# Kernel optimization log

Measured on AMD Instinct MI355X. Metric: run time of the kernel, lower is better.

## Reference

```python
import jax, jax.numpy as jnp
import numpy as np

T, B, C, H, K = 2048, 4, 1024, 16, 7  # timesteps, batch, channels, heads, kernel
R = C // H  # channels per head


def setup_inputs() -> dict:
    key = jax.random.key(0)
    k1, k2 = jax.random.split(key)
    x = jax.random.normal(k1, (T, B, C), dtype=jnp.float32)
    # xavier_uniform for weight_linear: shape (H*K, C), fan_in=C, fan_out=H*K
    a = float(np.sqrt(6.0 / (C + H * K)))
    W = jax.random.uniform(k2, (H * K, C), dtype=jnp.float32, minval=-a, maxval=a)
    conv_bias = jnp.zeros((C,), dtype=jnp.float32)
    return {"x": x, "W": W, "conv_bias": conv_bias}


def reference(x, W, conv_bias):
    Tn, Bn, Cn = x.shape
    Kn, Hn = K, H
    Rn = Cn // Hn
    # dynamic filters predicted from the input itself (query = x)
    w = jnp.einsum('tbc,oc->tbo', x, W).reshape(Tn, Bn, Hn, Kn)
    w = jax.nn.softmax(w, axis=-1)  # softmax over the small kernel dim
    # causal unfold: padding_l = K-1 zeros on the left of the time axis
    x_pad = jnp.pad(x, ((Kn - 1, 0), (0, 0), (0, 0)))
    # x_unf[t, b, c, k] = x[t - (K-1) + k]  (zeros outside)
    x_unf = jnp.stack([x_pad[k:k + Tn] for k in range(Kn)], axis=-1)  # T,B,C,K
    x_unf = x_unf.reshape(Tn, Bn, Hn, Rn, Kn)
    out = jnp.einsum('tbhrk,tbhk->tbhr', x_unf, w).reshape(Tn, Bn, Cn)
    return out + conv_bias[None, None, :]
```

## Files before the change

kernel.cpp:

```cpp
#include <hip/hip_runtime.h>
#include <hip/hip_bf16.h>

#define T_DIM 2048
#define B_DIM 4
#define C_DIM 1024
#define H_DIM 16
#define K_DIM 7
#define HK    112

typedef float f32x4 __attribute__((ext_vector_type(4)));
typedef short s16x8 __attribute__((ext_vector_type(8)));

__device__ __forceinline__ short f2bf(float f) {
    union { float f; unsigned u; } v; v.f = f;
    return (short)((v.u + 0x7FFFu + ((v.u >> 16) & 1u)) >> 16);
}

__global__ void k_cvtW(const float* __restrict__ W, short* __restrict__ Wb) {
    const int i = ((int)blockIdx.x * 256 + (int)threadIdx.x) * 8;
    f32x4 a = *(const f32x4*)(W + i);
    f32x4 b = *(const f32x4*)(W + i + 4);
    s16x8 o;
    o[0] = f2bf(a[0]); o[1] = f2bf(a[1]); o[2] = f2bf(a[2]); o[3] = f2bf(a[3]);
    o[4] = f2bf(b[0]); o[5] = f2bf(b[1]); o[6] = f2bf(b[2]); o[7] = f2bf(b[3]);
    *(s16x8*)(Wb + i) = o;
}

__global__ __launch_bounds__(256) void k_fused(const float* __restrict__ x,
                                               const short* __restrict__ Wb,
                                               const float* __restrict__ bias,
                                               float* __restrict__ out) {
    __shared__ float sm[4][16][113];
    __shared__ float smw[16][HK];

    const int tid  = (int)threadIdx.x;
    const int lane = tid & 63;
    const int wid  = tid >> 6;
    const int m0   = (int)blockIdx.x * 16;
    const int t0   = (int)blockIdx.x * 4;

    const int cl   = lane & 15;
    const int koff = (lane >> 4) * 8;

    const float* aptr = x  + (size_t)(m0 + cl) * C_DIM + koff;
    const short* bptr = Wb + (size_t)cl * C_DIM + koff;

    f32x4 acc[K_DIM];
    #pragma unroll
    for (int n = 0; n < K_DIM; ++n) acc[n] = (f32x4){0.f, 0.f, 0.f, 0.f};

    for (int q = 0; q < 8; ++q) {
        const int kb = wid * 8 + q;
        f32x4 a0 = *(const f32x4*)(aptr + kb * 32);
        f32x4 a1 = *(const f32x4*)(aptr + kb * 32 + 4);
        s16x8 afr;
        afr[0] = f2bf(a0[0]); afr[1] = f2bf(a0[1]); afr[2] = f2bf(a0[2]); afr[3] = f2bf(a0[3]);
        afr[4] = f2bf(a1[0]); afr[5] = f2bf(a1[1]); afr[6] = f2bf(a1[2]); afr[7] = f2bf(a1[3]);
        #pragma unroll
        for (int nt = 0; nt < K_DIM; ++nt) {
            s16x8 bf = *(const s16x8*)(bptr + nt * 16 * C_DIM + kb * 32);
            acc[nt] = __builtin_amdgcn_mfma_f32_16x16x32_bf16(afr, bf, acc[nt], 0, 0, 0);
        }
    }

    const int r0 = (lane >> 4) * 4;
    #pragma unroll
    for (int nt = 0; nt < K_DIM; ++nt)
        #pragma unroll
        for (int j = 0; j < 4; ++j)
            sm[wid][r0 + j][nt * 16 + cl] = acc[nt][j];
    __syncthreads();

    {
        const int r = tid >> 4, h = tid & 15;
        float v[K_DIM];
        float mx = -1e30f;
        #pragma unroll
        for (int k = 0; k < K_DIM; ++k) {
            v[k] = sm[0][r][h * 7 + k] + sm[1][r][h * 7 + k]
                 + sm[2][r][h * 7 + k] + sm[3][r][h * 7 + k];
            mx = fmaxf(mx, v[k]);
        }
        float s = 0.f;
        #pragma unroll
        for (int k = 0; k < K_DIM; ++k) { v[k] = __expf(v[k] - mx); s += v[k]; }
        const float inv = 1.f / s;
        #pragma unroll
        for (int k = 0; k < K_DIM; ++k) smw[r][h * 7 + k] = v[k] * inv;
    }
    __syncthreads();

    const int c4 = tid * 4;
    const int h  = tid >> 4;
    const f32x4 bias4 = *(const f32x4*)(bias + c4);
    const f32x4 zero4 = {0.f, 0.f, 0.f, 0.f};

    #pragma unroll
    for (int b = 0; b < B_DIM; ++b) {
        f32x4 rv[10];
        #pragma unroll
        for (int j = 0; j < 10; ++j) {
            const int t = t0 - 6 + j;
            rv[j] = (t >= 0)
                  ? *(const f32x4*)(x + (size_t)(t * B_DIM + b) * C_DIM + c4)
                  : zero4;
        }
        #pragma unroll
        for (int tt = 0; tt < 4; ++tt) {
            const float* wr = &smw[tt * 4 + b][h * 7];
            f32x4 o = bias4;
            o += rv[tt + 0] * wr[0];
            o += rv[tt + 1] * wr[1];
            o += rv[tt + 2] * wr[2];
            o += rv[tt + 3] * wr[3];
            o += rv[tt + 4] * wr[4];
            o += rv[tt + 5] * wr[5];
            o += rv[tt + 6] * wr[6];
            *(f32x4*)(out + (size_t)((t0 + tt) * B_DIM + b) * C_DIM + c4) = o;
        }
    }
}

extern "C" void kernel_launch(void* const* d_in, const int* in_sizes, int n_in,
                              void* d_out, int out_size, void* d_ws, size_t ws_size,
                              hipStream_t stream) {
    const float* x    = (const float*)d_in[0];
    const float* W    = (const float*)d_in[1];
    const float* bias = (const float*)d_in[2];
    float* out = (float*)d_out;
    short* Wb  = (short*)d_ws;

    k_cvtW <<<56, 256, 0, stream>>>(W, Wb);
    k_fused<<<(T_DIM * B_DIM) / 16, 256, 0, stream>>>(x, Wb, bias, out);
}
```

Baseline: 111.5 us.

## Use 512-thread blocks with split-K over 8 waves and early prefetch of conv inputs

The block grows from 256 to 512 threads, so the K-reduction of the filter GEMM is split across 8 waves instead of 4, with an 8-way shared-memory reduction. In the conv phase each half of the block handles two batch entries instead of one thread looping over all four. The first batch's 10-step input window is loaded before the GEMM to hide its latency, while the second is loaded after the softmax. The aim is more parallelism per block and overlap of global loads with MFMA work, at the cost of higher register pressure and more shared memory.

```diff
diff --git a/kernel.cpp b/kernel.cpp
--- a/kernel.cpp
+++ b/kernel.cpp
@@ -26,11 +26,11 @@
     *(s16x8*)(Wb + i) = o;
 }
 
-__global__ __launch_bounds__(256) void k_fused(const float* __restrict__ x,
-                                               const short* __restrict__ Wb,
-                                               const float* __restrict__ bias,
-                                               float* __restrict__ out) {
-    __shared__ float sm[4][16][113];
+__global__ __launch_bounds__(512, 4) void k_fused(const float* __restrict__ x,
+                                                  const short* __restrict__ Wb,
+                                                  const float* __restrict__ bias,
+                                                  float* __restrict__ out) {
+    __shared__ float sm[8][16][113];
     __shared__ float smw[16][HK];
 
     const int tid  = (int)threadIdx.x;
@@ -38,6 +38,21 @@
     const int wid  = tid >> 6;
     const int m0   = (int)blockIdx.x * 16;
     const int t0   = (int)blockIdx.x * 4;
+
+    const int cid = tid & 255;
+    const int bs2 = (tid >> 8) * 2;
+    const int c4  = cid * 4;
+    const int h   = cid >> 4;
+    const f32x4 zero4 = {0.f, 0.f, 0.f, 0.f};
+
+    f32x4 rv0[10];
+    #pragma unroll
+    for (int j = 0; j < 10; ++j) {
+        const int t = t0 - 6 + j;
+        rv0[j] = (t >= 0)
+               ? *(const f32x4*)(x + (size_t)(t * B_DIM + bs2) * C_DIM + c4)
+               : zero4;
+    }
 
     const int cl   = lane & 15;
     const int koff = (lane >> 4) * 8;
@@ -49,16 +64,16 @@
     #pragma unroll
     for (int n = 0; n < K_DIM; ++n) acc[n] = (f32x4){0.f, 0.f, 0.f, 0.f};
 
-    for (int q = 0; q < 8; ++q) {
-        const int kb = wid * 8 + q;
-        f32x4 a0 = *(const f32x4*)(aptr + kb * 32);
-        f32x4 a1 = *(const f32x4*)(aptr + kb * 32 + 4);
+    for (int q = 0; q < 4; ++q) {
+        const int kb32 = (wid * 4 + q) * 32;
+        f32x4 a0 = *(const f32x4*)(aptr + kb32);
+        f32x4 a1 = *(const f32x4*)(aptr + kb32 + 4);
         s16x8 afr;
         afr[0] = f2bf(a0[0]); afr[1] = f2bf(a0[1]); afr[2] = f2bf(a0[2]); afr[3] = f2bf(a0[3]);
         afr[4] = f2bf(a1[0]); afr[5] = f2bf(a1[1]); afr[6] = f2bf(a1[2]); afr[7] = f2bf(a1[3]);
         #pragma unroll
         for (int nt = 0; nt < K_DIM; ++nt) {
-            s16x8 bf = *(const s16x8*)(bptr + nt * 16 * C_DIM + kb * 32);
+            s16x8 bf = *(const s16x8*)(bptr + nt * 16 * C_DIM + kb32);
             acc[nt] = __builtin_amdgcn_mfma_f32_16x16x32_bf16(afr, bf, acc[nt], 0, 0, 0);
         }
     }
@@ -71,14 +86,15 @@
             sm[wid][r0 + j][nt * 16 + cl] = acc[nt][j];
     __syncthreads();
 
-    {
-        const int r = tid >> 4, h = tid & 15;
+    if (tid < 256) {
+        const int r = tid >> 4, hh = tid & 15;
         float v[K_DIM];
         float mx = -1e30f;
         #pragma unroll
         for (int k = 0; k < K_DIM; ++k) {
-            v[k] = sm[0][r][h * 7 + k] + sm[1][r][h * 7 + k]
-                 + sm[2][r][h * 7 + k] + sm[3][r][h * 7 + k];
+            const int cc = hh * 7 + k;
+            v[k] = ((sm[0][r][cc] + sm[1][r][cc]) + (sm[2][r][cc] + sm[3][r][cc]))
+                 + ((sm[4][r][cc] + sm[5][r][cc]) + (sm[6][r][cc] + sm[7][r][cc]));
             mx = fmaxf(mx, v[k]);
         }
         float s = 0.f;
@@ -86,38 +102,46 @@
         for (int k = 0; k < K_DIM; ++k) { v[k] = __expf(v[k] - mx); s += v[k]; }
         const float inv = 1.f / s;
         #pragma unroll
-        for (int k = 0; k < K_DIM; ++k) smw[r][h * 7 + k] = v[k] * inv;
+        for (int k = 0; k < K_DIM; ++k) smw[r][hh * 7 + k] = v[k] * inv;
     }
     __syncthreads();
 
-    const int c4 = tid * 4;
-    const int h  = tid >> 4;
     const f32x4 bias4 = *(const f32x4*)(bias + c4);
-    const f32x4 zero4 = {0.f, 0.f, 0.f, 0.f};
+
+    f32x4 rv1[10];
+    #pragma unroll
+    for (int j = 0; j < 10; ++j) {
+        const int t = t0 - 6 + j;
+        rv1[j] = (t >= 0)
+               ? *(const f32x4*)(x + (size_t)(t * B_DIM + bs2 + 1) * C_DIM + c4)
+               : zero4;
+    }
 
     #pragma unroll
-    for (int b = 0; b < B_DIM; ++b) {
-        f32x4 rv[10];
-        #pragma unroll
-        for (int j = 0; j < 10; ++j) {
-            const int t = t0 - 6 + j;
-            rv[j] = (t >= 0)
-                  ? *(const f32x4*)(x + (size_t)(t * B_DIM + b) * C_DIM + c4)
-                  : zero4;
-        }
-        #pragma unroll
-        for (int tt = 0; tt < 4; ++tt) {
-            const float* wr = &smw[tt * 4 + b][h * 7];
-            f32x4 o = bias4;
-            o += rv[tt + 0] * wr[0];
-            o += rv[tt + 1] * wr[1];
-            o += rv[tt + 2] * wr[2];
-            o += rv[tt + 3] * wr[3];
-            o += rv[tt + 4] * wr[4];
-            o += rv[tt + 5] * wr[5];
-            o += rv[tt + 6] * wr[6];
-            *(f32x4*)(out + (size_t)((t0 + tt) * B_DIM + b) * C_DIM + c4) = o;
-        }
+    for (int tt = 0; tt < 4; ++tt) {
+        const float* wr = &smw[tt * 4 + bs2][h * 7];
+        f32x4 o = bias4;
+        o += rv0[tt + 0] * wr[0];
+        o += rv0[tt + 1] * wr[1];
+        o += rv0[tt + 2] * wr[2];
+        o += rv0[tt + 3] * wr[3];
+        o += rv0[tt + 4] * wr[4];
+        o += rv0[tt + 5] * wr[5];
+        o += rv0[tt + 6] * wr[6];
+        *(f32x4*)(out + (size_t)((t0 + tt) * B_DIM + bs2) * C_DIM + c4) = o;
+    }
+    #pragma unroll
+    for (int tt = 0; tt < 4; ++tt) {
+        const float* wr = &smw[tt * 4 + bs2 + 1][h * 7];
+        f32x4 o = bias4;
+        o += rv1[tt + 0] * wr[0];
+        o += rv1[tt + 1] * wr[1];
+        o += rv1[tt + 2] * wr[2];
+        o += rv1[tt + 3] * wr[3];
+        o += rv1[tt + 4] * wr[4];
+        o += rv1[tt + 5] * wr[5];
+        o += rv1[tt + 6] * wr[6];
+        *(f32x4*)(out + (size_t)((t0 + tt) * B_DIM + bs2 + 1) * C_DIM + c4) = o;
     }
 }
 
@@ -131,5 +155,5 @@
     short* Wb  = (short*)d_ws;
 
     k_cvtW <<<56, 256, 0, stream>>>(W, Wb);
-    k_fused<<<(T_DIM * B_DIM) / 16, 256, 0, stream>>>(x, Wb, bias, out);
+    k_fused<<<(T_DIM * B_DIM) / 16, 512, 0, stream>>>(x, Wb, bias, out);
 }
```

Result: faster. 108.3 us (-2.9%).
